# Kernel optimization log

Measured on AMD Instinct MI355X. Metric: run time of the kernel, lower is better.

## Reference

```python
import jax, jax.numpy as jnp
import numpy as np

# Model dims (match init_kwargs cfg)
B, C_IN, L = 16, 3, 1024
D_MODEL, N_LAYERS = 256, 4
D_STATE, D_CONV, EXPAND = 16, 4, 2
D_INNER = EXPAND * D_MODEL            # 512
DT_RANK = (D_MODEL + 15) // 16        # 16 (mamba_ssm 'auto' rank)


def setup_inputs() -> dict:
    key = jax.random.key(0)
    ks = jax.random.split(key, 10)
    def rn(k, shape, scale):
        return jax.random.normal(k, shape, jnp.float32) * scale
    inp = {
        "x": jax.random.normal(ks[0], (B, C_IN, L), jnp.float32),
        # input stem: Conv1d(3 -> d_model, k=3, pad=1)
        "stem_w": rn(ks[1], (D_MODEL, C_IN, 3), 0.3),
        "stem_b": jnp.zeros((D_MODEL,), jnp.float32),
        # per-layer params, stacked on leading layer dim
        "norm_g": jnp.ones((N_LAYERS, D_MODEL), jnp.float32),
        "norm_b": jnp.zeros((N_LAYERS, D_MODEL), jnp.float32),
        "in_proj_w": rn(ks[2], (N_LAYERS, 2 * D_INNER, D_MODEL), 0.02),
        "conv_w": rn(ks[3], (N_LAYERS, D_INNER, D_CONV), 0.2),
        "conv_b": jnp.zeros((N_LAYERS, D_INNER), jnp.float32),
        "x_proj_w": rn(ks[4], (N_LAYERS, DT_RANK + 2 * D_STATE, D_INNER), 0.02),
        "dt_w": rn(ks[5], (N_LAYERS, D_INNER, DT_RANK), 0.05),
        "dt_b": jnp.full((N_LAYERS, D_INNER), -4.6, jnp.float32),  # softplus ~= 0.01
        "A_log": jnp.log(jnp.broadcast_to(
            jnp.arange(1, D_STATE + 1, dtype=jnp.float32), (N_LAYERS, D_INNER, D_STATE))),
        "Dp": jnp.ones((N_LAYERS, D_INNER), jnp.float32),
        "out_w": rn(ks[6], (N_LAYERS, D_MODEL, D_INNER), 0.02),
        # final norm + output head Conv1d(d_model -> 1, k=1)
        "fnorm_g": jnp.ones((D_MODEL,), jnp.float32),
        "fnorm_b": jnp.zeros((D_MODEL,), jnp.float32),
        "head_w": rn(ks[7], (1, D_MODEL), 0.05),
        "head_b": jnp.zeros((1,), jnp.float32),
    }
    return inp


def _layernorm(x, g, b, eps=1e-5):
    mu = jnp.mean(x, axis=-1, keepdims=True)
    var = jnp.mean((x - mu) ** 2, axis=-1, keepdims=True)
    return (x - mu) * jax.lax.rsqrt(var + eps) * g + b


def _silu(x):
    return x * jax.nn.sigmoid(x)


def _selective_scan(u, delta, A, Bm, Cm, D):
    # u, delta: [B, L, di]; Bm, Cm: [B, L, ds]; A: [di, ds]; D: [di]
    # h_t = exp(delta_t * A) * h_{t-1} + (delta_t * u_t) * B_t ; y_t = <C_t, h_t>
    def step(h, t):
        d_t, B_t, C_t, u_t = t  # [B,di], [B,ds], [B,ds], [B,di]
        h = h * jnp.exp(d_t[..., None] * A) + (d_t * u_t)[..., None] * B_t[:, None, :]
        return h, jnp.einsum('bds,bs->bd', h, C_t)
    h0 = jnp.zeros((u.shape[0], A.shape[0], A.shape[1]), u.dtype)
    xs = (jnp.moveaxis(delta, 1, 0), jnp.moveaxis(Bm, 1, 0),
          jnp.moveaxis(Cm, 1, 0), jnp.moveaxis(u, 1, 0))
    _, ys = jax.lax.scan(step, h0, xs)            # ys: [L, B, di]
    return jnp.moveaxis(ys, 0, 1) + u * D


def _mamba(x, in_w, cw, cb, xw, dtw, dtb, A_log, Dp, ow):
    # x: [B, L, d_model]
    xz = jnp.einsum('bld,ed->ble', x, in_w)       # [B, L, 2*di]
    xin, z = jnp.split(xz, 2, axis=-1)
    # causal depthwise conv over time
    xc = jnp.moveaxis(xin, 1, 2)                  # [B, di, L]
    xc = jax.lax.conv_general_dilated(
        xc, cw[:, None, :], (1,), [(D_CONV - 1, 0)],
        feature_group_count=D_INNER,
        dimension_numbers=('NCH', 'OIH', 'NCH')) + cb[None, :, None]
    xin = _silu(jnp.moveaxis(xc, 1, 2))           # [B, L, di]
    proj = jnp.einsum('bld,ed->ble', xin, xw)     # [B, L, dt_rank + 2*ds]
    dt = proj[..., :DT_RANK]
    Bm = proj[..., DT_RANK:DT_RANK + D_STATE]
    Cm = proj[..., DT_RANK + D_STATE:]
    delta = jax.nn.softplus(jnp.einsum('blr,dr->bld', dt, dtw) + dtb)
    A = -jnp.exp(A_log)
    y = _selective_scan(xin, delta, A, Bm, Cm, Dp)
    y = y * _silu(z)
    return jnp.einsum('bld,od->blo', y, ow)       # [B, L, d_model]


def reference(x, stem_w, stem_b, norm_g, norm_b, in_proj_w, conv_w, conv_b,
              x_proj_w, dt_w, dt_b, A_log, Dp, out_w, fnorm_g, fnorm_b,
              head_w, head_b):
    # stem: Conv1d(k=3, same padding) + ReLU
    h = jax.lax.conv_general_dilated(
        x, stem_w, (1,), [(1, 1)],
        dimension_numbers=('NCH', 'OIH', 'NCH')) + stem_b[None, :, None]
    h = jax.nn.relu(h)
    h = jnp.moveaxis(h, 1, 2)                     # [B, L, d_model]
    for i in range(N_LAYERS):
        h = h + _mamba(_layernorm(h, norm_g[i], norm_b[i]),
                       in_proj_w[i], conv_w[i], conv_b[i], x_proj_w[i],
                       dt_w[i], dt_b[i], A_log[i], Dp[i], out_w[i])
    h = _layernorm(h, fnorm_g, fnorm_b)
    out = jnp.einsum('bld,od->blo', h, head_w) + head_b
    return jax.nn.sigmoid(jnp.moveaxis(out, 1, 2))  # [B, 1, L]
```

## Files before the change

kernel.cpp:

```cpp
#include <hip/hip_runtime.h>
#include <math.h>

#define BSZ 16
#define LQ 1024
#define DM 256
#define DI 512
#define NT (BSZ*LQ)

typedef __attribute__((ext_vector_type(8))) short short8;
typedef __attribute__((ext_vector_type(4))) short short4v;
typedef __attribute__((ext_vector_type(4))) float f32x4;

#define AS1(p) (const __attribute__((address_space(1))) void*)(p)
#define AS3(p) (__attribute__((address_space(3))) void*)(p)
#define GLOAD16(g, l) __builtin_amdgcn_global_load_lds(AS1(g), AS3(l), 16, 0, 0)

__device__ __forceinline__ short f2bf(float f) {
  union { float f; unsigned u; } a; a.f = f;
  unsigned r = (a.u + 0x7FFF + ((a.u >> 16) & 1)) >> 16;
  return (short)r;
}
__device__ __forceinline__ float bf2f(short s) {
  union { unsigned u; float f; } a; a.u = ((unsigned)(unsigned short)s) << 16;
  return a.f;
}

__global__ void stem_kernel(const float* __restrict__ x, const float* __restrict__ w,
                            const float* __restrict__ bias, short* __restrict__ h) {
  int idx = blockIdx.x * 256 + threadIdx.x;
  int d = idx & 255;
  int l = (idx >> 8) & 1023;
  int b = idx >> 18;
  float acc = bias[d];
#pragma unroll
  for (int c = 0; c < 3; c++) {
    const float* xr = x + (size_t)(b * 3 + c) * LQ;
    const float* wr = w + (size_t)(d * 3 + c) * 3;
#pragma unroll
    for (int k = 0; k < 3; k++) {
      int t = l + k - 1;
      if (t >= 0 && t < LQ) acc += xr[t] * wr[k];
    }
  }
  h[idx] = f2bf(fmaxf(acc, 0.f));
}

#define WB_IN 262144
#define WB_XP 32768
#define WB_OUT 131072
#define WB_L (WB_IN + WB_XP + WB_OUT)

__global__ void convert_w(const float* __restrict__ in_w, const float* __restrict__ xp_w,
                          const float* __restrict__ out_w, short* __restrict__ wb) {
  int layer = blockIdx.y;
  int idx = blockIdx.x * 256 + threadIdx.x;
  short* dst = wb + (size_t)layer * WB_L;
  float v;
  if (idx < WB_IN) {
    v = in_w[(size_t)layer * WB_IN + idx];
  } else if (idx < WB_IN + WB_XP) {
    int k = idx - WB_IN; int row = k >> 9, col = k & 511;
    v = (row < 48) ? xp_w[(size_t)layer * 48 * 512 + row * 512 + col] : 0.f;
  } else {
    int k = idx - WB_IN - WB_XP;
    v = out_w[(size_t)layer * WB_OUT + k];
  }
  dst[idx] = f2bf(v);
}

__global__ void ln_kernel(const short* __restrict__ x, const float* __restrict__ g,
                          const float* __restrict__ bv, short* __restrict__ o) {
  int token = blockIdx.x * 4 + (threadIdx.x >> 6);
  int lane = threadIdx.x & 63;
  short4v xv = *(const short4v*)(x + (size_t)token * DM + lane * 4);
  f32x4 v;
#pragma unroll
  for (int k = 0; k < 4; k++) v[k] = bf2f(xv[k]);
  float s = v[0] + v[1] + v[2] + v[3];
  float q = v[0]*v[0] + v[1]*v[1] + v[2]*v[2] + v[3]*v[3];
#pragma unroll
  for (int off = 32; off > 0; off >>= 1) {
    s += __shfl_xor(s, off, 64);
    q += __shfl_xor(q, off, 64);
  }
  float mu = s * (1.f / DM);
  float var = q * (1.f / DM) - mu * mu;
  float rs = rsqrtf(var + 1e-5f);
  f32x4 gg = *(const f32x4*)(g + lane * 4);
  f32x4 bb = *(const f32x4*)(bv + lane * 4);
  short4v ov;
#pragma unroll
  for (int k = 0; k < 4; k++) ov[k] = f2bf((v[k] - mu) * rs * gg[k] + bb[k]);
  *(short4v*)(o + (size_t)token * DM + lane * 4) = ov;
}

__global__ __launch_bounds__(256) void gemm_mfma_s16(
    const short* __restrict__ A, int K,
    const short* __restrict__ W,
    short* __restrict__ C0, int ld0,
    short* __restrict__ C1, int ld1,
    int split, int N) {
  __shared__ short As[2][128 * 32];
  __shared__ short Bs[2][128 * 32];
  int tid = threadIdx.x;
  int wave = tid >> 6, lane = tid & 63;
  int bm = blockIdx.y * 128, bn = blockIdx.x * 128;
  int wm = (wave >> 1) * 64, wn = (wave & 1) * 64;

  f32x4 acc[4][4];
#pragma unroll
  for (int i = 0; i < 4; i++)
#pragma unroll
    for (int j = 0; j < 4; j++) { acc[i][j][0]=0.f; acc[i][j][1]=0.f; acc[i][j][2]=0.f; acc[i][j][3]=0.f; }

  int srow = lane >> 2;
  int scol = (lane & 3) * 8;
  const short* Ag = A + (size_t)(bm + wave * 32 + srow) * K + scol;
  const short* Wg = W + (size_t)(bn + wave * 32 + srow) * K + scol;
  short* As0W = As[0] + wave * 32 * 32;
  short* As1W = As[1] + wave * 32 * 32;
  short* Bs0W = Bs[0] + wave * 32 * 32;
  short* Bs1W = Bs[1] + wave * 32 * 32;

  int fr = lane & 15;
  int kg = (lane >> 4) * 8;

  for (int k0 = 0; k0 < K; k0 += 64) {
    GLOAD16(Ag + k0,                         As0W);
    GLOAD16(Ag + k0 + (size_t)16 * K,        As0W + 16 * 32);
    GLOAD16(Ag + k0 + 32,                    As1W);
    GLOAD16(Ag + k0 + 32 + (size_t)16 * K,   As1W + 16 * 32);
    GLOAD16(Wg + k0,                         Bs0W);
    GLOAD16(Wg + k0 + (size_t)16 * K,        Bs0W + 16 * 32);
    GLOAD16(Wg + k0 + 32,                    Bs1W);
    GLOAD16(Wg + k0 + 32 + (size_t)16 * K,   Bs1W + 16 * 32);
    __syncthreads();

#pragma unroll
    for (int ks = 0; ks < 2; ks++) {
      short8 af[4], bf[4];
#pragma unroll
      for (int i = 0; i < 4; i++) af[i] = *(const short8*)&As[ks][(wm + i * 16 + fr) * 32 + kg];
#pragma unroll
      for (int j = 0; j < 4; j++) bf[j] = *(const short8*)&Bs[ks][(wn + j * 16 + fr) * 32 + kg];
#pragma unroll
      for (int i = 0; i < 4; i++)
#pragma unroll
        for (int j = 0; j < 4; j++)
          acc[i][j] = __builtin_amdgcn_mfma_f32_16x16x32_bf16(bf[j], af[i], acc[i][j], 0, 0, 0);
    }
    __syncthreads();
  }

  int tn = lane & 15, cr = (lane >> 4) * 4;
#pragma unroll
  for (int i = 0; i < 4; i++) {
    int token = bm + wm + i * 16 + tn;
#pragma unroll
    for (int j = 0; j < 4; j++) {
      int col0 = bn + wn + j * 16 + cr;
      short4v ov;
#pragma unroll
      for (int r = 0; r < 4; r++) ov[r] = f2bf(acc[i][j][r]);
      short* p = (col0 < split) ? (C0 + (size_t)token * ld0 + col0)
                                : (C1 + (size_t)token * ld1 + (col0 - split));
      *(short4v*)p = ov;
    }
  }
}

__global__ __launch_bounds__(256) void gemm2_conv(
    const short* __restrict__ xcb, const float* __restrict__ cw, const float* __restrict__ cb,
    const short* __restrict__ W, short* __restrict__ xinb, float* __restrict__ proj) {
  __shared__ short As[32 * 72];
  __shared__ short Bs[64 * 64];
  __shared__ float sCW[512 * 4];
  __shared__ float sCB[512];
  int tid = threadIdx.x;
  int wave = tid >> 6, lane = tid & 63;
  int bm = blockIdx.y * 32;
  int wm = (wave >> 1) * 16, wn = (wave & 1) * 32;

  for (int i = tid; i < 2048; i += 256) sCW[i] = cw[i];
  for (int i = tid; i < 512; i += 256) sCB[i] = cb[i];
  __syncthreads();

  f32x4 acc[2];
  acc[0] = (f32x4){0.f,0.f,0.f,0.f};
  acc[1] = (f32x4){0.f,0.f,0.f,0.f};

  int fr = lane & 15, kg = (lane >> 4) * 8;
  int r = tid >> 3;
  int cg = (tid & 7) * 8;
  int t = bm + r;
  int l = t & 1023;

  for (int k0 = 0; k0 < 512; k0 += 64) {
#pragma unroll
    for (int i = 0; i < 2; i++) {
      int c = tid + i * 256;
      GLOAD16(W + (size_t)(c >> 3) * 512 + k0 + (c & 7) * 8, Bs + c * 8);
    }
    int ch0 = k0 + cg;
    short8 xv[4];
#pragma unroll
    for (int k = 0; k < 4; k++) {
      if (l + k - 3 >= 0) xv[k] = *(const short8*)(xcb + (size_t)(t + k - 3) * 512 + ch0);
      else xv[k] = (short8)0;
    }
    short8 ov;
#pragma unroll
    for (int e = 0; e < 8; e++) {
      f32x4 wv = *(const f32x4*)&sCW[(ch0 + e) * 4];
      float a = sCB[ch0 + e];
#pragma unroll
      for (int k = 0; k < 4; k++) a += bf2f(xv[k][e]) * wv[k];
      a = a / (1.f + __expf(-a));
      ov[e] = f2bf(a);
    }
    *(short8*)&As[r * 72 + cg] = ov;
    *(short8*)(xinb + (size_t)t * 512 + ch0) = ov;
    __syncthreads();

#pragma unroll
    for (int ks = 0; ks < 2; ks++) {
      short8 af = *(const short8*)&As[(wm + fr) * 72 + ks * 32 + kg];
#pragma unroll
      for (int j = 0; j < 2; j++) {
        short8 bf = *(const short8*)&Bs[(wn + j * 16 + fr) * 64 + ks * 32 + kg];
        acc[j] = __builtin_amdgcn_mfma_f32_16x16x32_bf16(af, bf, acc[j], 0, 0, 0);
      }
    }
    __syncthreads();
  }

  int cn = lane & 15, cr = (lane >> 4) * 4;
  int row0 = bm + wm + cr;
#pragma unroll
  for (int j = 0; j < 2; j++) {
    int col = wn + j * 16 + cn;
    if (col < 48) {
#pragma unroll
      for (int rr2 = 0; rr2 < 4; rr2++)
        proj[(size_t)(row0 + rr2) * 48 + col] = acc[j][rr2];
    }
  }
}

__global__ __launch_bounds__(256) void gemm_mfma64(
    const short* __restrict__ A, int K,
    const short* __restrict__ W,
    short* __restrict__ C, int ldc, int N, int accum) {
  __shared__ short As[64 * 64];
  __shared__ short Bs[64 * 64];
  int tid = threadIdx.x;
  int wave = tid >> 6, lane = tid & 63;
  int bm = blockIdx.y * 64, bn = blockIdx.x * 64;
  int wm = (wave >> 1) * 32, wn = (wave & 1) * 32;

  f32x4 acc[2][2];
#pragma unroll
  for (int i = 0; i < 2; i++)
#pragma unroll
    for (int j = 0; j < 2; j++) { acc[i][j][0]=0.f; acc[i][j][1]=0.f; acc[i][j][2]=0.f; acc[i][j][3]=0.f; }

  const short* Ag = A + (size_t)bm * K;
  const short* Wg = W + (size_t)bn * K;
  int fr = lane & 15;
  int kg = (lane >> 4) * 8;

  for (int k0 = 0; k0 < K; k0 += 64) {
#pragma unroll
    for (int i = 0; i < 2; i++) {
      int c = tid + i * 256;
      int row = c >> 3, kk = (c & 7) * 8;
      GLOAD16(Ag + (size_t)row * K + k0 + kk, As + c * 8);
      GLOAD16(Wg + (size_t)row * K + k0 + kk, Bs + c * 8);
    }
    __syncthreads();

#pragma unroll
    for (int ks = 0; ks < 2; ks++) {
      short8 af[2], bf[2];
#pragma unroll
      for (int i = 0; i < 2; i++) af[i] = *(const short8*)&As[(wm + i * 16 + fr) * 64 + ks * 32 + kg];
#pragma unroll
      for (int j = 0; j < 2; j++) bf[j] = *(const short8*)&Bs[(wn + j * 16 + fr) * 64 + ks * 32 + kg];
#pragma unroll
      for (int i = 0; i < 2; i++)
#pragma unroll
        for (int j = 0; j < 2; j++)
          acc[i][j] = __builtin_amdgcn_mfma_f32_16x16x32_bf16(bf[j], af[i], acc[i][j], 0, 0, 0);
    }
    __syncthreads();
  }

  int tn = lane & 15, cr = (lane >> 4) * 4;
#pragma unroll
  for (int i = 0; i < 2; i++) {
    int token = bm + wm + i * 16 + tn;
#pragma unroll
    for (int j = 0; j < 2; j++) {
      int col0 = bn + wn + j * 16 + cr;
      if (col0 < N) {
        short* p = C + (size_t)token * ldc + col0;
        short4v ov;
        if (accum) {
          short4v old = *(const short4v*)p;
#pragma unroll
          for (int r = 0; r < 4; r++) ov[r] = f2bf(acc[i][j][r] + bf2f(old[r]));
        } else {
#pragma unroll
          for (int r = 0; r < 4; r++) ov[r] = f2bf(acc[i][j][r]);
        }
        *(short4v*)p = ov;
      }
    }
  }
}

template <int CTRL>
__device__ __forceinline__ float dpp_add(float x) {
  int yi = __builtin_amdgcn_update_dpp(0, __float_as_int(x), CTRL, 0xF, 0xF, true);
  return x + __int_as_float(yi);
}
__device__ __forceinline__ float sum16(float x) {
  x = dpp_add<0xB1>(x);
  x = dpp_add<0x4E>(x);
  x = dpp_add<0x124>(x);
  x = dpp_add<0x128>(x);
  return x;
}

#define TCH 32
__global__ __launch_bounds__(256) void scan_kernel(
    const short* __restrict__ xinb, const float* __restrict__ proj,
    const short* __restrict__ zc,
    const float* __restrict__ dt_w, const float* __restrict__ dt_b,
    const float* __restrict__ A_log, const float* __restrict__ Dp,
    short* __restrict__ ybf) {
  int b  = blockIdx.x >> 5;
  int d0 = (blockIdx.x & 31) << 4;
  int tid = threadIdx.x;
  int ci = tid >> 4;
  int s  = tid & 15;
  int d = d0 + ci;

  __shared__ float sDt[32 * 20];
  __shared__ float sBT[16 * 36];
  __shared__ float sCT[16 * 36];
  __shared__ float sUT[16 * 36];
  __shared__ float sDU[16 * 36];
  __shared__ float sDel[16 * 36];
  __shared__ float sY[32 * 17];

  float Av = -__expf(A_log[(size_t)d * 16 + s]);
  f32x4 wv4[4];
#pragma unroll
  for (int k = 0; k < 4; k++) wv4[k] = *(const f32x4*)&dt_w[(size_t)d * 16 + k * 4];
  float db = dt_b[d];
  float Ddj = Dp[d0 + s];
  float h = 0.f;

  const float* projb = proj + (size_t)b * LQ * 48;
  const short* xinbb = xinb + (size_t)b * LQ * 512 + d0;
  const short* zcb   = zc   + (size_t)b * LQ * 512 + d0;
  short* ybb         = ybf  + (size_t)b * LQ * 512 + d0;

  int tt = tid >> 4, j = tid & 15;

  int tr[6], rr[6];
#pragma unroll
  for (int k = 0; k < 6; k++) { int idx = tid + k * 256; tr[k] = idx / 48; rr[k] = idx - tr[k] * 48; }

  float uv0, uv1, zv0, zv1;
  {
    float pjv[6];
#pragma unroll
    for (int k = 0; k < 6; k++) pjv[k] = projb[tid + k * 256];
    uv0 = bf2f(xinbb[(size_t)tt * 512 + j]);
    uv1 = bf2f(xinbb[(size_t)(tt + 16) * 512 + j]);
    zv0 = bf2f(zcb[(size_t)tt * 512 + j]);
    zv1 = bf2f(zcb[(size_t)(tt + 16) * 512 + j]);
#pragma unroll
    for (int k = 0; k < 6; k++) {
      int r = rr[k], t = tr[k];
      if (r < 16)      sDt[t * 20 + r] = pjv[k];
      else if (r < 32) sBT[(r - 16) * 36 + t] = pjv[k];
      else             sCT[(r - 32) * 36 + t] = pjv[k];
    }
    sUT[j * 36 + tt] = uv0;
    sUT[j * 36 + tt + 16] = uv1;
  }
  __syncthreads();

  const int NCH = LQ / TCH;
  for (int c = 0; c < NCH; c++) {
    int t0 = c * TCH;

    float pjn[6], un0 = 0.f, un1 = 0.f, zn0 = 0.f, zn1 = 0.f;
    if (c + 1 < NCH) {
      const float* g = projb + (t0 + TCH) * 48;
#pragma unroll
      for (int k = 0; k < 6; k++) pjn[k] = g[tid + k * 256];
      un0 = bf2f(xinbb[(size_t)(t0 + TCH + tt) * 512 + j]);
      un1 = bf2f(xinbb[(size_t)(t0 + TCH + tt + 16) * 512 + j]);
      zn0 = bf2f(zcb[(size_t)(t0 + TCH + tt) * 512 + j]);
      zn1 = bf2f(zcb[(size_t)(t0 + TCH + tt + 16) * 512 + j]);
    }

    {
      f32x4 a0 = *(const f32x4*)&sDt[s * 20 + 0];
      f32x4 a1 = *(const f32x4*)&sDt[s * 20 + 4];
      f32x4 a2 = *(const f32x4*)&sDt[s * 20 + 8];
      f32x4 a3 = *(const f32x4*)&sDt[s * 20 + 12];
      f32x4 b0 = *(const f32x4*)&sDt[(s + 16) * 20 + 0];
      f32x4 b1 = *(const f32x4*)&sDt[(s + 16) * 20 + 4];
      f32x4 b2 = *(const f32x4*)&sDt[(s + 16) * 20 + 8];
      f32x4 b3 = *(const f32x4*)&sDt[(s + 16) * 20 + 12];
      float dt0 = db, dt1 = db;
#pragma unroll
      for (int q = 0; q < 4; q++) {
        dt0 += a0[q] * wv4[0][q] + a1[q] * wv4[1][q] + a2[q] * wv4[2][q] + a3[q] * wv4[3][q];
        dt1 += b0[q] * wv4[0][q] + b1[q] * wv4[1][q] + b2[q] * wv4[2][q] + b3[q] * wv4[3][q];
      }
      float de0 = (dt0 > 15.f) ? dt0 : __logf(1.f + __expf(dt0));
      float de1 = (dt1 > 15.f) ? dt1 : __logf(1.f + __expf(dt1));
      float u0 = sUT[ci * 36 + s];
      float u1 = sUT[ci * 36 + s + 16];
      sDel[ci * 36 + s]      = de0;
      sDel[ci * 36 + s + 16] = de1;
      sDU[ci * 36 + s]       = de0 * u0;
      sDU[ci * 36 + s + 16]  = de1 * u1;
    }
    __syncthreads();

    {
      float ee[TCH], cin[TCH];
      f32x4 ct[8];
      {
        f32x4 dl[8], du8[8], bt[8];
#pragma unroll
        for (int k = 0; k < 8; k++) {
          dl[k]  = *(const f32x4*)&sDel[ci * 36 + k * 4];
          du8[k] = *(const f32x4*)&sDU[ci * 36 + k * 4];
          bt[k]  = *(const f32x4*)&sBT[s * 36 + k * 4];
          ct[k]  = *(const f32x4*)&sCT[s * 36 + k * 4];
        }
#pragma unroll
        for (int t = 0; t < TCH; t++) {
          ee[t] = __expf(dl[t >> 2][t & 3] * Av);
          cin[t] = du8[t >> 2][t & 3] * bt[t >> 2][t & 3];
        }
      }
      float pv0 = 0.f, pv1 = 0.f;
#pragma unroll
      for (int t = 0; t < TCH; t++) {
        h = h * ee[t] + cin[t];
        float p = sum16(h * ct[t >> 2][t & 3]);
        if (t < 16) pv0 = (s == t) ? p : pv0;
        else        pv1 = (s == (t - 16)) ? p : pv1;
      }
      sY[s * 17 + ci] = pv0;
      sY[(s + 16) * 17 + ci] = pv1;
    }
    __syncthreads();

    {
      float p0 = sY[tt * 17 + j];
      float p1 = sY[(tt + 16) * 17 + j];
      float y0 = p0 + uv0 * Ddj;
      float y1 = p1 + uv1 * Ddj;
      float g0 = zv0 / (1.f + __expf(-zv0));
      float g1 = zv1 / (1.f + __expf(-zv1));
      ybb[(size_t)(t0 + tt) * 512 + j] = f2bf(y0 * g0);
      ybb[(size_t)(t0 + tt + 16) * 512 + j] = f2bf(y1 * g1);
    }
    if (c + 1 < NCH) {
#pragma unroll
      for (int k = 0; k < 6; k++) {
        int r = rr[k], t = tr[k];
        if (r < 16)      sDt[t * 20 + r] = pjn[k];
        else if (r < 32) sBT[(r - 16) * 36 + t] = pjn[k];
        else             sCT[(r - 32) * 36 + t] = pjn[k];
      }
      sUT[j * 36 + tt] = un0;
      sUT[j * 36 + tt + 16] = un1;
      uv0 = un0; uv1 = un1; zv0 = zn0; zv1 = zn1;
    }
    __syncthreads();
  }
}

__global__ void head_kernel(const short* __restrict__ h, const float* __restrict__ g,
                            const float* __restrict__ bv, const float* __restrict__ hw,
                            const float* __restrict__ hb, float* __restrict__ out) {
  int token = blockIdx.x * 4 + (threadIdx.x >> 6);
  int lane = threadIdx.x & 63;
  short4v xv = *(const short4v*)(h + (size_t)token * DM + lane * 4);
  f32x4 v;
#pragma unroll
  for (int k = 0; k < 4; k++) v[k] = bf2f(xv[k]);
  float s = v[0] + v[1] + v[2] + v[3];
  float q = v[0]*v[0] + v[1]*v[1] + v[2]*v[2] + v[3]*v[3];
#pragma unroll
  for (int off = 32; off > 0; off >>= 1) {
    s += __shfl_xor(s, off, 64);
    q += __shfl_xor(q, off, 64);
  }
  float mu = s * (1.f / DM);
  float rs = rsqrtf(q * (1.f / DM) - mu * mu + 1e-5f);
  f32x4 gg = *(const f32x4*)(g + lane * 4);
  f32x4 bb = *(const f32x4*)(bv + lane * 4);
  f32x4 ww = *(const f32x4*)(hw + lane * 4);
  float c = 0.f;
#pragma unroll
  for (int k = 0; k < 4; k++) c += ((v[k] - mu) * rs * gg[k] + bb[k]) * ww[k];
#pragma unroll
  for (int off = 32; off > 0; off >>= 1) c += __shfl_xor(c, off, 64);
  if (lane == 0) out[token] = 1.f / (1.f + __expf(-(c + hb[0])));
}

extern "C" void kernel_launch(void* const* d_in, const int* in_sizes, int n_in,
                              void* d_out, int out_size, void* d_ws, size_t ws_size,
                              hipStream_t stream) {
  const float* x        = (const float*)d_in[0];
  const float* stem_w   = (const float*)d_in[1];
  const float* stem_b   = (const float*)d_in[2];
  const float* norm_g   = (const float*)d_in[3];
  const float* norm_b   = (const float*)d_in[4];
  const float* in_proj_w= (const float*)d_in[5];
  const float* conv_w   = (const float*)d_in[6];
  const float* conv_b   = (const float*)d_in[7];
  const float* x_proj_w = (const float*)d_in[8];
  const float* dt_w     = (const float*)d_in[9];
  const float* dt_b     = (const float*)d_in[10];
  const float* A_log    = (const float*)d_in[11];
  const float* Dp       = (const float*)d_in[12];
  const float* out_w    = (const float*)d_in[13];
  const float* fnorm_g  = (const float*)d_in[14];
  const float* fnorm_b  = (const float*)d_in[15];
  const float* head_w   = (const float*)d_in[16];
  const float* head_b   = (const float*)d_in[17];

  char* base = (char*)d_ws;
  short* h    = (short*)(base);
  short* xcb  = (short*)(base + ((size_t)16 << 20));
  short* zcb  = (short*)(base + ((size_t)32 << 20));
  short* xnb  = (short*)(base + ((size_t)48 << 20));
  short* xinb = (short*)(base + ((size_t)56 << 20));
  short* ybf  = (short*)(base + ((size_t)72 << 20));
  float* proj = (float*)(base + ((size_t)88 << 20));
  short* wb   = (short*)(base + ((size_t)91 << 20));

  stem_kernel<<<NT, 256, 0, stream>>>(x, stem_w, stem_b, h);

  dim3 gcw(WB_L / 256, 4);
  convert_w<<<gcw, 256, 0, stream>>>(in_proj_w, x_proj_w, out_w, wb);

  for (int i = 0; i < 4; i++) {
    const short* wbl = wb + (size_t)i * WB_L;

    ln_kernel<<<NT / 4, 256, 0, stream>>>(h, norm_g + i * DM, norm_b + i * DM, xnb);

    dim3 g1(8, NT / 128);
    gemm_mfma_s16<<<g1, 256, 0, stream>>>(xnb, 256, wbl, xcb, 512, zcb, 512, 512, 1024);

    dim3 g2(1, NT / 32);
    gemm2_conv<<<g2, 256, 0, stream>>>(xcb, conv_w + i * DI * 4, conv_b + i * DI,
                                       wbl + WB_IN, xinb, proj);

    scan_kernel<<<512, 256, 0, stream>>>(xinb, proj, zcb,
                                         dt_w + (size_t)i * DI * 16, dt_b + i * DI,
                                         A_log + (size_t)i * DI * 16, Dp + i * DI, ybf);

    dim3 g3(4, NT / 64);
    gemm_mfma64<<<g3, 256, 0, stream>>>(ybf, 512, wbl + WB_IN + WB_XP, h, 256, 256, 1);
  }

  head_kernel<<<NT / 4, 256, 0, stream>>>(h, fnorm_g, fnorm_b, head_w, head_b, (float*)d_out);
}
```

Before: 720.5 us.

## Compute scan output contraction with bf16 MFMA instead of DPP reductions

```diff
diff --git a/kernel.cpp b/kernel.cpp
--- a/kernel.cpp
+++ b/kernel.cpp
@@ -19,6 +19,10 @@
   union { float f; unsigned u; } a; a.f = f;
   unsigned r = (a.u + 0x7FFF + ((a.u >> 16) & 1)) >> 16;
   return (short)r;
+}
+__device__ __forceinline__ short bfr(float f) {
+  union { float f; unsigned u; } a; a.f = f;
+  return (short)((a.u + 0x8000u) >> 16);
 }
 __device__ __forceinline__ float bf2f(short s) {
   union { unsigned u; float f; } a; a.u = ((unsigned)(unsigned short)s) << 16;
@@ -319,20 +323,9 @@
   }
 }
 
-template <int CTRL>
-__device__ __forceinline__ float dpp_add(float x) {
-  int yi = __builtin_amdgcn_update_dpp(0, __float_as_int(x), CTRL, 0xF, 0xF, true);
-  return x + __int_as_float(yi);
-}
-__device__ __forceinline__ float sum16(float x) {
-  x = dpp_add<0xB1>(x);
-  x = dpp_add<0x4E>(x);
-  x = dpp_add<0x124>(x);
-  x = dpp_add<0x128>(x);
-  return x;
-}
-
 #define TCH 32
+#define HST 20
+#define HCS (32*HST + 8)
 __global__ __launch_bounds__(256) void scan_kernel(
     const short* __restrict__ xinb, const float* __restrict__ proj,
     const short* __restrict__ zc,
@@ -348,10 +341,11 @@
 
   __shared__ float sDt[32 * 20];
   __shared__ float sBT[16 * 36];
-  __shared__ float sCT[16 * 36];
+  __shared__ short sCb[32 * HST];
   __shared__ float sUT[16 * 36];
   __shared__ float sDU[16 * 36];
   __shared__ float sDel[16 * 36];
+  __shared__ short sH[16 * HCS];
   __shared__ float sY[32 * 17];
 
   float Av = -__expf(A_log[(size_t)d * 16 + s]);
@@ -368,6 +362,10 @@
   short* ybb         = ybf  + (size_t)b * LQ * 512 + d0;
 
   int tt = tid >> 4, j = tid & 15;
+  int lane = tid & 63;
+  int q = lane >> 4;
+  int m = lane & 15;
+  int wbase = (tid >> 6) << 2;
 
   int tr[6], rr[6];
 #pragma unroll
@@ -387,7 +385,7 @@
       int r = rr[k], t = tr[k];
       if (r < 16)      sDt[t * 20 + r] = pjv[k];
       else if (r < 32) sBT[(r - 16) * 36 + t] = pjv[k];
-      else             sCT[(r - 32) * 36 + t] = pjv[k];
+      else             sCb[t * HST + (r - 32)] = f2bf(pjv[k]);
     }
     sUT[j * 36 + tt] = uv0;
     sUT[j * 36 + tt + 16] = uv1;
@@ -420,9 +418,9 @@
       f32x4 b3 = *(const f32x4*)&sDt[(s + 16) * 20 + 12];
       float dt0 = db, dt1 = db;
 #pragma unroll
-      for (int q = 0; q < 4; q++) {
-        dt0 += a0[q] * wv4[0][q] + a1[q] * wv4[1][q] + a2[q] * wv4[2][q] + a3[q] * wv4[3][q];
-        dt1 += b0[q] * wv4[0][q] + b1[q] * wv4[1][q] + b2[q] * wv4[2][q] + b3[q] * wv4[3][q];
+      for (int qq = 0; qq < 4; qq++) {
+        dt0 += a0[qq] * wv4[0][qq] + a1[qq] * wv4[1][qq] + a2[qq] * wv4[2][qq] + a3[qq] * wv4[3][qq];
+        dt1 += b0[qq] * wv4[0][qq] + b1[qq] * wv4[1][qq] + b2[qq] * wv4[2][qq] + b3[qq] * wv4[3][qq];
       }
       float de0 = (dt0 > 15.f) ? dt0 : __logf(1.f + __expf(dt0));
       float de1 = (dt1 > 15.f) ? dt1 : __logf(1.f + __expf(dt1));
@@ -435,34 +433,51 @@
     }
     __syncthreads();
 
-    {
-      float ee[TCH], cin[TCH];
-      f32x4 ct[8];
+#pragma unroll
+    for (int hf = 0; hf < 2; hf++) {
+      float ee[16], cin[16];
       {
-        f32x4 dl[8], du8[8], bt[8];
-#pragma unroll
-        for (int k = 0; k < 8; k++) {
-          dl[k]  = *(const f32x4*)&sDel[ci * 36 + k * 4];
-          du8[k] = *(const f32x4*)&sDU[ci * 36 + k * 4];
-          bt[k]  = *(const f32x4*)&sBT[s * 36 + k * 4];
-          ct[k]  = *(const f32x4*)&sCT[s * 36 + k * 4];
+        f32x4 dl[4], du8[4], bt[4];
+#pragma unroll
+        for (int k = 0; k < 4; k++) {
+          dl[k]  = *(const f32x4*)&sDel[ci * 36 + hf * 16 + k * 4];
+          du8[k] = *(const f32x4*)&sDU[ci * 36 + hf * 16 + k * 4];
+          bt[k]  = *(const f32x4*)&sBT[s * 36 + hf * 16 + k * 4];
         }
 #pragma unroll
-        for (int t = 0; t < TCH; t++) {
+        for (int t = 0; t < 16; t++) {
           ee[t] = __expf(dl[t >> 2][t & 3] * Av);
           cin[t] = du8[t >> 2][t & 3] * bt[t >> 2][t & 3];
         }
       }
-      float pv0 = 0.f, pv1 = 0.f;
-#pragma unroll
-      for (int t = 0; t < TCH; t++) {
+#pragma unroll
+      for (int t = 0; t < 16; t++) {
         h = h * ee[t] + cin[t];
-        float p = sum16(h * ct[t >> 2][t & 3]);
-        if (t < 16) pv0 = (s == t) ? p : pv0;
-        else        pv1 = (s == (t - 16)) ? p : pv1;
-      }
-      sY[s * 17 + ci] = pv0;
-      sY[(s + 16) * 17 + ci] = pv1;
+        sH[ci * HCS + (hf * 16 + t) * HST + s] = bfr(h);
+      }
+      short8 cf = (short8)0;
+      if (q < 2) {
+        short4v lo = *(const short4v*)&sCb[(hf * 16 + m) * HST + q * 8];
+        short4v hi = *(const short4v*)&sCb[(hf * 16 + m) * HST + q * 8 + 4];
+        cf = (short8){lo[0],lo[1],lo[2],lo[3],hi[0],hi[1],hi[2],hi[3]};
+      }
+#pragma unroll
+      for (int cc = 0; cc < 4; cc++) {
+        int cw = wbase + cc;
+        short8 hfr = (short8)0;
+        if (q < 2) {
+          short4v lo = *(const short4v*)&sH[cw * HCS + (hf * 16 + m) * HST + q * 8];
+          short4v hi = *(const short4v*)&sH[cw * HCS + (hf * 16 + m) * HST + q * 8 + 4];
+          hfr = (short8){lo[0],lo[1],lo[2],lo[3],hi[0],hi[1],hi[2],hi[3]};
+        }
+        f32x4 Dv = __builtin_amdgcn_mfma_f32_16x16x32_bf16(cf, hfr,
+                       (f32x4){0.f,0.f,0.f,0.f}, 0, 0, 0);
+        if ((m >> 2) == q) {
+          int rsel = m & 3;
+          float dv = (rsel == 0) ? Dv[0] : (rsel == 1) ? Dv[1] : (rsel == 2) ? Dv[2] : Dv[3];
+          sY[(hf * 16 + m) * 17 + cw] = dv;
+        }
+      }
     }
     __syncthreads();
 
@@ -482,7 +497,7 @@
         int r = rr[k], t = tr[k];
         if (r < 16)      sDt[t * 20 + r] = pjn[k];
         else if (r < 32) sBT[(r - 16) * 36 + t] = pjn[k];
-        else             sCT[(r - 32) * 36 + t] = pjn[k];
+        else             sCb[t * HST + (r - 32)] = f2bf(pjn[k]);
       }
       sUT[j * 36 + tt] = un0;
       sUT[j * 36 + tt + 16] = un1;
```

Measured after the change: 797.8 us. +10.7%, slower.
